# Optimization experiments

Hardware: AMD Instinct MI355X
Metric: run time of the kernel (lower is better)

The kernel has to match this reference:

```python
import jax, jax.numpy as jnp
import numpy as np
from jax import lax

B, T, F = 64, 1536, 512
POOL = 6
UNITS = 256
NUM_CLASSES = 250


def _hard_sigmoid(x):
    # Keras hard_sigmoid: clip(0.2*x + 0.5, 0, 1)
    return jnp.clip(0.2 * x + 0.5, 0.0, 1.0)


def setup_inputs() -> dict:
    key = jax.random.key(0)
    ks = jax.random.split(key, 6)
    x = jax.random.normal(ks[0], (B, T, F), dtype=jnp.float32)
    # ConvLSTM1D with kernel_size=1 over a length-1 spatial axis == dense gates.
    W = jax.random.normal(ks[1], (F, 4 * UNITS), dtype=jnp.float32) * 0.05   # input kernel
    R = jax.random.normal(ks[2], (UNITS, 4 * UNITS), dtype=jnp.float32) * 0.05  # recurrent kernel
    b = jnp.zeros((4 * UNITS,), dtype=jnp.float32)
    Wd = jax.random.normal(ks[3], (UNITS, NUM_CLASSES), dtype=jnp.float32) * 0.05
    bd = jnp.zeros((NUM_CLASSES,), dtype=jnp.float32)
    return {"x": x, "W": W, "R": R, "b": b, "Wd": Wd, "bd": bd}


def reference(x, W, R, b, Wd, bd):
    Bx, Tx, Fx = x.shape
    Tp = Tx // POOL
    # AveragePooling1D(pool_size=6) over time
    xp = x[:, : Tp * POOL].reshape(Bx, Tp, POOL, Fx).mean(axis=2)  # [B, Tp, F]
    # Precompute input-to-gate contribution for all steps (one big GEMM)
    zx = jnp.einsum('btf,fg->btg', xp, W) + b  # [B, Tp, 4U]
    z_seq = jnp.swapaxes(zx, 0, 1)  # [Tp, B, 4U]

    h0 = jnp.zeros((Bx, UNITS), dtype=x.dtype)
    c0 = jnp.zeros((Bx, UNITS), dtype=x.dtype)

    def step(carry, z_t):
        h, c = carry
        z = z_t + h @ R  # [B, 4U]
        i, f, g, o = jnp.split(z, 4, axis=-1)  # Keras gate order: i, f, c, o
        i = _hard_sigmoid(i)
        f = _hard_sigmoid(f)
        g = jnp.tanh(g)
        o = _hard_sigmoid(o)
        c = f * c + i * g
        h = o * jnp.tanh(c)
        return (h, c), None

    (h, _), _ = lax.scan(step, (h0, c0), z_seq)
    # squeeze(-2) + dropout(eval: identity) + flatten -> [B, UNITS]
    logits = h @ Wd + bd
    return jax.nn.softmax(logits, axis=-1)
```

## Files before the change

kernel.cpp:

```cpp
#include <hip/hip_runtime.h>
#include <hip/hip_bf16.h>

#define BB 64
#define TT 1536
#define FF 512
#define TP 256
#define UU 256
#define GG 1024
#define NC 250

typedef _Float16 h2_t __attribute__((ext_vector_type(2)));
typedef _Float16 f16x8 __attribute__((ext_vector_type(8)));
typedef float f32x4 __attribute__((ext_vector_type(4)));

#if defined(__has_builtin)
#  if __has_builtin(__builtin_amdgcn_fdot2)
#    define FDOT2(a, b, c) __builtin_amdgcn_fdot2((a), (b), (c), false)
#  endif
#endif
#ifndef FDOT2
__device__ __forceinline__ float fdot2_fb(h2_t a, h2_t b, float c) {
    return c + (float)a[0] * (float)b[0] + (float)a[1] * (float)b[1];
}
#  define FDOT2(a, b, c) fdot2_fb((a), (b), (c))
#endif

#define BC(u) __builtin_bit_cast(h2_t, (u))

__device__ __forceinline__ float hsig(float z) {
    return fminf(fmaxf(fmaf(z, 0.2f, 0.5f), 0.0f), 1.0f);
}

__device__ __forceinline__ float ftanh(float x) {
    float ax = fabsf(x);
    float e = __expf(-2.0f * ax);
    float t = (1.0f - e) / (1.0f + e);
    return copysignf(t, x);
}

__device__ __forceinline__ void dot4(float& z, const uint4& r, const uint4& h) {
    z = FDOT2(BC(r.x), BC(h.x), z);
    z = FDOT2(BC(r.y), BC(h.y), z);
    z = FDOT2(BC(r.z), BC(h.z), z);
    z = FDOT2(BC(r.w), BC(h.w), z);
}

#if defined(__has_builtin) && __has_builtin(__builtin_amdgcn_mov_dpp)
template <int CTRL>
__device__ __forceinline__ float qperm(float v) {
    return __builtin_bit_cast(float,
        __builtin_amdgcn_mov_dpp(__builtin_bit_cast(int, v), CTRL, 0xf, 0xf, true));
}
#else
template <int CTRL>
__device__ __forceinline__ float qperm(float v) {
    return __shfl_xor(v, CTRL == 0xB1 ? 1 : 2, 64);
}
#endif

__global__ __launch_bounds__(256) void pool_kernel(const float* __restrict__ x,
                                                   _Float16* __restrict__ xph) {
    int idx = blockIdx.x * 256 + threadIdx.x;
    int f4 = (idx & 127) << 2;
    int m = idx >> 7;
    int tp = m & (TP - 1);
    int b = m >> 8;
    const float* src = x + ((size_t)b * TT + (size_t)tp * 6) * FF + f4;
    float sx = 0.f, sy = 0.f, sz = 0.f, sw = 0.f;
#pragma unroll
    for (int j = 0; j < 6; ++j) {
        float4 v = *(const float4*)&src[j * FF];
        sx += v.x; sy += v.y; sz += v.z; sw += v.w;
    }
    const float r6 = 1.0f / 6.0f;
    h2_t lo, hi;
    lo[0] = (_Float16)(sx * r6); lo[1] = (_Float16)(sy * r6);
    hi[0] = (_Float16)(sz * r6); hi[1] = (_Float16)(sw * r6);
    float2 w = make_float2(__builtin_bit_cast(float, lo), __builtin_bit_cast(float, hi));
    *(float2*)&xph[(size_t)m * FF + f4] = w;
}

template <int PERM>
__global__ __launch_bounds__(256) void transpose_cvt(const float* __restrict__ in,
                                                     _Float16* __restrict__ out,
                                                     int K, int N) {
    __shared__ _Float16 tile[32][42];
    const int r = threadIdx.x >> 3;
    const int c4 = (threadIdx.x & 7) << 2;
    const int n0 = blockIdx.x << 5;
    const int k0 = blockIdx.y << 5;
    float4 v = *(const float4*)&in[(size_t)(k0 + r) * N + n0 + c4];
    tile[r][c4 + 0] = (_Float16)v.x;
    tile[r][c4 + 1] = (_Float16)v.y;
    tile[r][c4 + 2] = (_Float16)v.z;
    tile[r][c4 + 3] = (_Float16)v.w;
    __syncthreads();
    int n = n0 + r;
    int orow = PERM ? (((n & 255) << 2) | (n >> 8)) : n;
    h2_t lo, hi;
    lo[0] = tile[c4 + 0][r]; lo[1] = tile[c4 + 1][r];
    hi[0] = tile[c4 + 2][r]; hi[1] = tile[c4 + 3][r];
    float2 w = make_float2(__builtin_bit_cast(float, lo), __builtin_bit_cast(float, hi));
    *(float2*)&out[(size_t)orow * K + k0 + c4] = w;
}

__global__ __launch_bounds__(256) void conv_rq(const _Float16* __restrict__ Rt,
                                               uint4* __restrict__ Rq) {
    int d = blockIdx.x * 256 + threadIdx.x;
    int q = d >> 10, t = d & 1023;
    int g = q >> 3, kk = q & 7;
    int u = t >> 2, s = t & 3;
    int col = (g << 8) | u;
    int k0 = (s << 6) | (kk << 3);
    Rq[d] = *(const uint4*)&Rt[(size_t)col * 256 + k0];
}

__global__ __launch_bounds__(256, 2) void gemm_zx_mfma(const _Float16* __restrict__ Ah,
                                                       const _Float16* __restrict__ Bt,
                                                       const float* __restrict__ bias,
                                                       float* __restrict__ C) {
    __shared__ _Float16 As[128 * 40];
    __shared__ _Float16 Bs[128 * 40];
    const int tid = threadIdx.x;
    const int bn = blockIdx.x * 128;
    const int bm = blockIdx.y * 128;
    const int wave = tid >> 6, lane = tid & 63;
    const int wm = (wave & 1) * 64, wn = (wave >> 1) * 64;
    const int l15 = lane & 15, q8 = (lane >> 4) * 8;
    const int srow = tid >> 1, shalf = tid & 1;

    f32x4 acc[4][4] = {};
    const uint4* ag = (const uint4*)(Ah + (size_t)(bm + srow) * FF);
    const uint4* bg = (const uint4*)(Bt + (size_t)(bn + srow) * FF);
    uint4* as_st = (uint4*)As + 5 * srow + 2 * shalf;
    uint4* bs_st = (uint4*)Bs + 5 * srow + 2 * shalf;

    for (int k0 = 0; k0 < FF; k0 += 32) {
        int qi = (k0 >> 3) + shalf * 2;
        uint4 a0 = ag[qi], a1 = ag[qi + 1];
        uint4 b0 = bg[qi], b1 = bg[qi + 1];
        __syncthreads();
        as_st[0] = a0; as_st[1] = a1;
        bs_st[0] = b0; bs_st[1] = b1;
        __syncthreads();
        f16x8 af[4], bf[4];
#pragma unroll
        for (int mt = 0; mt < 4; ++mt)
            af[mt] = *(const f16x8*)&As[(wm + 16 * mt + l15) * 40 + q8];
#pragma unroll
        for (int nt = 0; nt < 4; ++nt)
            bf[nt] = *(const f16x8*)&Bs[(wn + 16 * nt + l15) * 40 + q8];
#pragma unroll
        for (int mt = 0; mt < 4; ++mt)
#pragma unroll
            for (int nt = 0; nt < 4; ++nt)
                acc[mt][nt] = __builtin_amdgcn_mfma_f32_16x16x32_f16(af[mt], bf[nt],
                                                                    acc[mt][nt], 0, 0, 0);
    }
    const int rq = (lane >> 4) * 4;
#pragma unroll
    for (int nt = 0; nt < 4; ++nt) {
        int col = bn + wn + 16 * nt + l15;
        int oc = ((col & 3) << 8) | (col >> 2);
        float bv = bias[oc];
#pragma unroll
        for (int mt = 0; mt < 4; ++mt) {
#pragma unroll
            for (int r = 0; r < 4; ++r) {
                int row = bm + wm + 16 * mt + rq + r;
                C[(size_t)row * GG + col] = ((const float*)&acc[mt][nt])[r] + bv;
            }
        }
    }
}

__global__ __launch_bounds__(1024) void lstm_scan(const float* __restrict__ zx,
                                                  const uint4* __restrict__ Rq,
                                                  float* __restrict__ hfin) {
    __shared__ uint4 Rl[9][1024];
    __shared__ __align__(16) _Float16 hbuf[2][4][72];
    const int b = blockIdx.x;
    const int t = threadIdx.x;
    const int u = t >> 2, s = t & 3;

    const uint4* rqt = Rq + t;

    uint4 rv0[6], rv1[6], rv2[6], rv3[5];
#pragma unroll
    for (int kk = 0; kk < 6; ++kk) {
        rv0[kk] = rqt[(0 * 8 + kk) * 1024];
        rv1[kk] = rqt[(1 * 8 + kk) * 1024];
        rv2[kk] = rqt[(2 * 8 + kk) * 1024];
        if (kk < 5) rv3[kk] = rqt[(3 * 8 + kk) * 1024];
    }
    Rl[0][t] = rqt[(0 * 8 + 6) * 1024];
    Rl[1][t] = rqt[(0 * 8 + 7) * 1024];
    Rl[2][t] = rqt[(1 * 8 + 6) * 1024];
    Rl[3][t] = rqt[(1 * 8 + 7) * 1024];
    Rl[4][t] = rqt[(2 * 8 + 6) * 1024];
    Rl[5][t] = rqt[(2 * 8 + 7) * 1024];
    Rl[6][t] = rqt[(3 * 8 + 5) * 1024];
    Rl[7][t] = rqt[(3 * 8 + 6) * 1024];
    Rl[8][t] = rqt[(3 * 8 + 7) * 1024];

    if (t < 288) ((unsigned*)hbuf)[t] = 0u;
    float c = 0.0f;
    const float4* zxp = (const float4*)zx + (size_t)b * TP * UU + u;
    float4 zn = zxp[0];
    __syncthreads();

#pragma unroll 1
    for (int step = 0; step < TP; ++step) {
        float4 zn2 = zxp[(size_t)((step + 1 < TP) ? step + 1 : step) * UU];
        const char* hbase = (const char*)hbuf[step & 1] + s * 144;
        float z0 = 0.f, z1 = 0.f, z2 = 0.f, z3 = 0.f;
#pragma unroll
        for (int kk = 0; kk < 8; ++kk) {
            uint4 hh = *(const uint4*)(hbase + kk * 16);
            if (kk < 6) dot4(z0, rv0[kk], hh); else dot4(z0, Rl[kk - 6][t], hh);
            if (kk < 6) dot4(z1, rv1[kk], hh); else dot4(z1, Rl[2 + kk - 6][t], hh);
            if (kk < 6) dot4(z2, rv2[kk], hh); else dot4(z2, Rl[4 + kk - 6][t], hh);
            if (kk < 5) dot4(z3, rv3[kk], hh); else dot4(z3, Rl[6 + kk - 5][t], hh);
        }
        z0 += qperm<0xB1>(z0); z0 += qperm<0x4E>(z0);
        z1 += qperm<0xB1>(z1); z1 += qperm<0x4E>(z1);
        z2 += qperm<0xB1>(z2); z2 += qperm<0x4E>(z2);
        z3 += qperm<0xB1>(z3); z3 += qperm<0x4E>(z3);

        float ig = hsig(z0 + zn.x);
        float fg = hsig(z1 + zn.y);
        float gv = ftanh(z2 + zn.z);
        float og = hsig(z3 + zn.w);
        c = fmaf(fg, c, ig * gv);
        float h = og * ftanh(c);
        if (s == 0) {
            hbuf[(step + 1) & 1][u >> 6][u & 63] = (_Float16)h;
            if (step == TP - 1) hfin[(size_t)b * UU + u] = h;
        }
        zn = zn2;
        __syncthreads();
    }
}

__global__ __launch_bounds__(256) void dense_softmax(const float* __restrict__ hfin,
                                                     const float* __restrict__ Wd,
                                                     const float* __restrict__ bd,
                                                     float* __restrict__ out) {
    __shared__ __align__(16) float hbuf[UU];
    __shared__ float red[256];
    const int b = blockIdx.x;
    const int tid = threadIdx.x;
    hbuf[tid] = hfin[(size_t)b * UU + tid];
    __syncthreads();
    float logit = -3.0e38f;
    if (tid < NC) {
        float acc = bd[tid];
        for (int u = 0; u < UU; u += 4) {
            float4 hv = *(const float4*)&hbuf[u];
            acc = fmaf(hv.x, Wd[(size_t)(u + 0) * NC + tid], acc);
            acc = fmaf(hv.y, Wd[(size_t)(u + 1) * NC + tid], acc);
            acc = fmaf(hv.z, Wd[(size_t)(u + 2) * NC + tid], acc);
            acc = fmaf(hv.w, Wd[(size_t)(u + 3) * NC + tid], acc);
        }
        logit = acc;
    }
    red[tid] = logit;
    __syncthreads();
    for (int sdx = 128; sdx > 0; sdx >>= 1) {
        if (tid < sdx) red[tid] = fmaxf(red[tid], red[tid + sdx]);
        __syncthreads();
    }
    float mx = red[0];
    __syncthreads();
    float e = (tid < NC) ? expf(logit - mx) : 0.0f;
    red[tid] = e;
    __syncthreads();
    for (int sdx = 128; sdx > 0; sdx >>= 1) {
        if (tid < sdx) red[tid] += red[tid + sdx];
        __syncthreads();
    }
    if (tid < NC) out[(size_t)b * NC + tid] = e / red[0];
}

extern "C" void kernel_launch(void* const* d_in, const int* in_sizes, int n_in,
                              void* d_out, int out_size, void* d_ws, size_t ws_size,
                              hipStream_t stream) {
    const float* x  = (const float*)d_in[0];
    const float* W  = (const float*)d_in[1];
    const float* R  = (const float*)d_in[2];
    const float* bv = (const float*)d_in[3];
    const float* Wd = (const float*)d_in[4];
    const float* bd = (const float*)d_in[5];
    float* out = (float*)d_out;

    char* ws = (char*)d_ws;
    _Float16* xph = (_Float16*)ws;
    float* zx = (float*)(ws + 16777216);
    _Float16* Rt = (_Float16*)(ws + 16777216);
    _Float16* Wtp = (_Float16*)(ws + 83886080);
    uint4* Rq = (uint4*)(ws + 84934656);
    float* hfin = (float*)(ws + 85458944);

    hipLaunchKernelGGL(pool_kernel, dim3(8192), dim3(256), 0, stream, x, xph);
    hipLaunchKernelGGL(HIP_KERNEL_NAME(transpose_cvt<1>), dim3(32, 16), dim3(256), 0,
                       stream, W, Wtp, FF, GG);
    hipLaunchKernelGGL(HIP_KERNEL_NAME(transpose_cvt<0>), dim3(32, 8), dim3(256), 0,
                       stream, R, Rt, UU, GG);
    hipLaunchKernelGGL(conv_rq, dim3(128), dim3(256), 0, stream, Rt, Rq);
    hipLaunchKernelGGL(gemm_zx_mfma, dim3(8, 128), dim3(256), 0, stream,
                       xph, Wtp, bv, zx);
    hipLaunchKernelGGL(lstm_scan, dim3(64), dim3(1024), 0, stream, zx, Rq, hfin);
    hipLaunchKernelGGL(dense_softmax, dim3(64), dim3(256), 0, stream, hfin, Wd, bd, out);
}
```

Baseline: 805.8 us.

## Split LSTM recurrence over 2 lanes per unit with DPP-swapped h chunks

The recurrent scan now uses 512 threads per batch row with each hidden unit split across 2 lanes (128 K each) instead of 4 lanes. Neighbouring lanes load alternating 16-byte h chunks and exchange them via a DPP swap, so each LDS read of h is reused for two weight chunks. The cross-lane reduction drops from two steps to one. The weight layout in conv_rq is reorganised to match. The cost is more registers per thread and extra DPP moves, with fewer waves available to hide latency in the serial loop.

```diff
diff --git a/kernel.cpp b/kernel.cpp
--- a/kernel.cpp
+++ b/kernel.cpp
@@ -51,12 +51,22 @@
     return __builtin_bit_cast(float,
         __builtin_amdgcn_mov_dpp(__builtin_bit_cast(int, v), CTRL, 0xf, 0xf, true));
 }
+__device__ __forceinline__ unsigned uswap2(unsigned v) {
+    return (unsigned)__builtin_amdgcn_mov_dpp((int)v, 0x4E, 0xf, 0xf, true);
+}
 #else
 template <int CTRL>
 __device__ __forceinline__ float qperm(float v) {
     return __shfl_xor(v, CTRL == 0xB1 ? 1 : 2, 64);
 }
+__device__ __forceinline__ unsigned uswap2(unsigned v) { return __shfl_xor(v, 2, 64); }
 #endif
+
+__device__ __forceinline__ uint4 swap2_quad(uint4 v) {
+    uint4 r;
+    r.x = uswap2(v.x); r.y = uswap2(v.y); r.z = uswap2(v.z); r.w = uswap2(v.w);
+    return r;
+}
 
 __global__ __launch_bounds__(256) void pool_kernel(const float* __restrict__ x,
                                                    _Float16* __restrict__ xph) {
@@ -107,11 +117,11 @@
 __global__ __launch_bounds__(256) void conv_rq(const _Float16* __restrict__ Rt,
                                                uint4* __restrict__ Rq) {
     int d = blockIdx.x * 256 + threadIdx.x;
-    int q = d >> 10, t = d & 1023;
-    int g = q >> 3, kk = q & 7;
-    int u = t >> 2, s = t & 3;
+    int q = d >> 9, t = d & 511;
+    int g = q >> 4, kk = q & 15;
+    int u = t >> 1, s = t & 1;
     int col = (g << 8) | u;
-    int k0 = (s << 6) | (kk << 3);
+    int k0 = (s << 7) | (kk << 3);
     Rq[d] = *(const uint4*)&Rt[(size_t)col * 256 + k0];
 }
 
@@ -174,34 +184,43 @@
     }
 }
 
-__global__ __launch_bounds__(1024) void lstm_scan(const float* __restrict__ zx,
-                                                  const uint4* __restrict__ Rq,
-                                                  float* __restrict__ hfin) {
-    __shared__ uint4 Rl[9][1024];
-    __shared__ __align__(16) _Float16 hbuf[2][4][72];
+__global__ __launch_bounds__(512) void lstm_scan(const float* __restrict__ zx,
+                                                 const uint4* __restrict__ Rq,
+                                                 float* __restrict__ hfin) {
+    __shared__ uint4 Rl[12][512];
+    __shared__ __align__(16) _Float16 hbuf[2][2][144];
     const int b = blockIdx.x;
     const int t = threadIdx.x;
-    const int u = t >> 2, s = t & 3;
+    const int u = t >> 1, s = t & 1, qs = u & 1;
 
     const uint4* rqt = Rq + t;
 
-    uint4 rv0[6], rv1[6], rv2[6], rv3[5];
-#pragma unroll
-    for (int kk = 0; kk < 6; ++kk) {
-        rv0[kk] = rqt[(0 * 8 + kk) * 1024];
-        rv1[kk] = rqt[(1 * 8 + kk) * 1024];
-        rv2[kk] = rqt[(2 * 8 + kk) * 1024];
-        if (kk < 5) rv3[kk] = rqt[(3 * 8 + kk) * 1024];
-    }
-    Rl[0][t] = rqt[(0 * 8 + 6) * 1024];
-    Rl[1][t] = rqt[(0 * 8 + 7) * 1024];
-    Rl[2][t] = rqt[(1 * 8 + 6) * 1024];
-    Rl[3][t] = rqt[(1 * 8 + 7) * 1024];
-    Rl[4][t] = rqt[(2 * 8 + 6) * 1024];
-    Rl[5][t] = rqt[(2 * 8 + 7) * 1024];
-    Rl[6][t] = rqt[(3 * 8 + 5) * 1024];
-    Rl[7][t] = rqt[(3 * 8 + 6) * 1024];
-    Rl[8][t] = rqt[(3 * 8 + 7) * 1024];
+    uint4 rE0[7], rO0[7], rE1[7], rO1[7], rE2[6], rO2[6], rE3[6], rO3[6];
+#pragma unroll
+    for (int j = 0; j < 7; ++j) {
+        rE0[j] = rqt[(size_t)(0 * 16 + 2 * j + qs) * 512];
+        rO0[j] = rqt[(size_t)(0 * 16 + 2 * j + 1 - qs) * 512];
+        rE1[j] = rqt[(size_t)(1 * 16 + 2 * j + qs) * 512];
+        rO1[j] = rqt[(size_t)(1 * 16 + 2 * j + 1 - qs) * 512];
+        if (j < 6) {
+            rE2[j] = rqt[(size_t)(2 * 16 + 2 * j + qs) * 512];
+            rO2[j] = rqt[(size_t)(2 * 16 + 2 * j + 1 - qs) * 512];
+            rE3[j] = rqt[(size_t)(3 * 16 + 2 * j + qs) * 512];
+            rO3[j] = rqt[(size_t)(3 * 16 + 2 * j + 1 - qs) * 512];
+        }
+    }
+    Rl[0][t]  = rqt[(size_t)(2 * 16 + 12 + qs) * 512];
+    Rl[1][t]  = rqt[(size_t)(2 * 16 + 13 - qs) * 512];
+    Rl[2][t]  = rqt[(size_t)(3 * 16 + 12 + qs) * 512];
+    Rl[3][t]  = rqt[(size_t)(3 * 16 + 13 - qs) * 512];
+    Rl[4][t]  = rqt[(size_t)(0 * 16 + 14 + qs) * 512];
+    Rl[5][t]  = rqt[(size_t)(0 * 16 + 15 - qs) * 512];
+    Rl[6][t]  = rqt[(size_t)(1 * 16 + 14 + qs) * 512];
+    Rl[7][t]  = rqt[(size_t)(1 * 16 + 15 - qs) * 512];
+    Rl[8][t]  = rqt[(size_t)(2 * 16 + 14 + qs) * 512];
+    Rl[9][t]  = rqt[(size_t)(2 * 16 + 15 - qs) * 512];
+    Rl[10][t] = rqt[(size_t)(3 * 16 + 14 + qs) * 512];
+    Rl[11][t] = rqt[(size_t)(3 * 16 + 15 - qs) * 512];
 
     if (t < 288) ((unsigned*)hbuf)[t] = 0u;
     float c = 0.0f;
@@ -212,20 +231,33 @@
 #pragma unroll 1
     for (int step = 0; step < TP; ++step) {
         float4 zn2 = zxp[(size_t)((step + 1 < TP) ? step + 1 : step) * UU];
-        const char* hbase = (const char*)hbuf[step & 1] + s * 144;
+        const char* hb = (const char*)hbuf + (step & 1) * 576 + s * 288 + qs * 16;
         float z0 = 0.f, z1 = 0.f, z2 = 0.f, z3 = 0.f;
 #pragma unroll
-        for (int kk = 0; kk < 8; ++kk) {
-            uint4 hh = *(const uint4*)(hbase + kk * 16);
-            if (kk < 6) dot4(z0, rv0[kk], hh); else dot4(z0, Rl[kk - 6][t], hh);
-            if (kk < 6) dot4(z1, rv1[kk], hh); else dot4(z1, Rl[2 + kk - 6][t], hh);
-            if (kk < 6) dot4(z2, rv2[kk], hh); else dot4(z2, Rl[4 + kk - 6][t], hh);
-            if (kk < 5) dot4(z3, rv3[kk], hh); else dot4(z3, Rl[6 + kk - 5][t], hh);
-        }
-        z0 += qperm<0xB1>(z0); z0 += qperm<0x4E>(z0);
-        z1 += qperm<0xB1>(z1); z1 += qperm<0x4E>(z1);
-        z2 += qperm<0xB1>(z2); z2 += qperm<0x4E>(z2);
-        z3 += qperm<0xB1>(z3); z3 += qperm<0x4E>(z3);
+        for (int j = 0; j < 8; ++j) {
+            uint4 ha = *(const uint4*)(hb + j * 32);
+            uint4 hx = swap2_quad(ha);
+            if (j < 6) {
+                dot4(z0, rE0[j], ha); dot4(z0, rO0[j], hx);
+                dot4(z1, rE1[j], ha); dot4(z1, rO1[j], hx);
+                dot4(z2, rE2[j], ha); dot4(z2, rO2[j], hx);
+                dot4(z3, rE3[j], ha); dot4(z3, rO3[j], hx);
+            } else if (j == 6) {
+                dot4(z0, rE0[6], ha);  dot4(z0, rO0[6], hx);
+                dot4(z1, rE1[6], ha);  dot4(z1, rO1[6], hx);
+                dot4(z2, Rl[0][t], ha); dot4(z2, Rl[1][t], hx);
+                dot4(z3, Rl[2][t], ha); dot4(z3, Rl[3][t], hx);
+            } else {
+                dot4(z0, Rl[4][t], ha);  dot4(z0, Rl[5][t], hx);
+                dot4(z1, Rl[6][t], ha);  dot4(z1, Rl[7][t], hx);
+                dot4(z2, Rl[8][t], ha);  dot4(z2, Rl[9][t], hx);
+                dot4(z3, Rl[10][t], ha); dot4(z3, Rl[11][t], hx);
+            }
+        }
+        z0 += qperm<0xB1>(z0);
+        z1 += qperm<0xB1>(z1);
+        z2 += qperm<0xB1>(z2);
+        z3 += qperm<0xB1>(z3);
 
         float ig = hsig(z0 + zn.x);
         float fg = hsig(z1 + zn.y);
@@ -234,7 +266,7 @@
         c = fmaf(fg, c, ig * gv);
         float h = og * ftanh(c);
         if (s == 0) {
-            hbuf[(step + 1) & 1][u >> 6][u & 63] = (_Float16)h;
+            hbuf[(step + 1) & 1][u >> 7][u & 127] = (_Float16)h;
             if (step == TP - 1) hfin[(size_t)b * UU + u] = h;
         }
         zn = zn2;
@@ -309,6 +341,6 @@
     hipLaunchKernelGGL(conv_rq, dim3(128), dim3(256), 0, stream, Rt, Rq);
     hipLaunchKernelGGL(gemm_zx_mfma, dim3(8, 128), dim3(256), 0, stream,
                        xph, Wtp, bv, zx);
-    hipLaunchKernelGGL(lstm_scan, dim3(64), dim3(1024), 0, stream, zx, Rq, hfin);
+    hipLaunchKernelGGL(lstm_scan, dim3(64), dim3(512), 0, stream, zx, Rq, hfin);
     hipLaunchKernelGGL(dense_softmax, dim3(64), dim3(256), 0, stream, hfin, Wd, bd, out);
 }
```

Result: faster. 720.2 us (-10.6%).
